# Performance work log

Hardware: AMD Instinct MI355X
Metric: run time of the kernel (lower is better)

The kernel has to match this reference:

```python
import jax, jax.numpy as jnp
import numpy as np

B, S, E = 2, 8192, 128


def setup_inputs() -> dict:
    key = jax.random.key(0)
    ks = jax.random.split(key, 7)
    sc = 1.0 / np.sqrt(E)
    return {
        "x": jax.random.normal(ks[0], (B, S, E), dtype=jnp.float32),
        "Wq": jax.random.normal(ks[1], (E, E), dtype=jnp.float32) * sc,
        "bq": jax.random.normal(ks[2], (E,), dtype=jnp.float32) * 0.01,
        "Wk": jax.random.normal(ks[3], (E, E), dtype=jnp.float32) * sc,
        "bk": jax.random.normal(ks[4], (E,), dtype=jnp.float32) * 0.01,
        "Wv": jax.random.normal(ks[5], (E, E), dtype=jnp.float32) * sc,
        "bv": jax.random.normal(ks[6], (E,), dtype=jnp.float32) * 0.01,
    }


def reference(x, Wq, bq, Wk, bk, Wv, bv):
    # x: [B, S, E]. Conv1d(k=1) == per-slice linear: out[b,s,o] = sum_e W[o,e] x[b,s,e] + b[o]
    embed_dim = x.shape[-1]
    Q = jnp.einsum("bse,oe->bso", x, Wq) + bq  # [B, S, E]
    K = jnp.einsum("bse,oe->bso", x, Wk) + bk
    V = jnp.einsum("bse,oe->bso", x, Wv) + bv
    scores = jnp.einsum("bsd,btd->bst", Q, K) / jnp.sqrt(
        jnp.asarray(embed_dim, dtype=x.dtype)
    )  # [B, S, S]
    A = jax.nn.softmax(scores, axis=-1)
    # torch: out = bmm(V^T_as[B,E,S], A^T)[.transpose] == sum_t A[b,s,t] V[b,t,e]
    out = jnp.einsum("bst,bte->bse", A, V)  # [B, S, E]
    return out
```

## Files before the change

kernel.cpp:

```cpp
#include <hip/hip_runtime.h>
#include <math.h>

#define NB 2
#define NS 8192
#define NE 128
#define NROWS (NB * NS)

typedef __attribute__((ext_vector_type(8))) short s8v;
typedef __attribute__((ext_vector_type(16))) float fx16;
typedef __attribute__((address_space(1))) const unsigned char as1c;
typedef __attribute__((address_space(3))) unsigned char as3t;

static __device__ __forceinline__ unsigned int pkbf(float a, float b) {
    unsigned int ua = __float_as_uint(a), ub = __float_as_uint(b);
    ua += 0x7FFFu + ((ua >> 16) & 1u);
    ub += 0x7FFFu + ((ub >> 16) & 1u);
    return (ua >> 16) | (ub & 0xFFFF0000u);
}

__global__ __launch_bounds__(256, 2)
void qkv_kernel(const float* __restrict__ x,
                const float* __restrict__ Wq, const float* __restrict__ bq,
                const float* __restrict__ Wk, const float* __restrict__ bk,
                const float* __restrict__ Wv, const float* __restrict__ bv,
                unsigned short* __restrict__ qkv)
{
    __shared__ unsigned short WhL[64 * 136];
    __shared__ unsigned short WlL[64 * 136];

    const int t    = threadIdx.x;
    const int rblk = blockIdx.x * 128;
    const int mat  = blockIdx.y;
    const int o0   = blockIdx.z * 64;

    const float* W    = (mat == 0) ? Wq : (mat == 1) ? Wk : Wv;
    const float* bias = (mat == 0) ? bq : (mat == 1) ? bk : bv;
    unsigned short* out = qkv + (size_t)mat * NROWS * NE;
    const float osc = (mat == 0) ? 0.08838834764831845f : 1.0f;

    {
        const int r = t >> 2, cg = (t & 3) * 32;
        #pragma unroll
        for (int j = 0; j < 4; ++j) {
            const float* wp = &W[(size_t)(o0 + r) * NE + cg + j * 8];
            float4 a = *(const float4*)wp;
            float4 b = *(const float4*)(wp + 4);
            unsigned int h0 = pkbf(a.x, a.y), h1 = pkbf(a.z, a.w);
            unsigned int h2 = pkbf(b.x, b.y), h3 = pkbf(b.z, b.w);
            *(uint4*)&WhL[r * 136 + cg + j * 8] = make_uint4(h0, h1, h2, h3);
            float l0 = a.x - __uint_as_float(h0 << 16);
            float l1 = a.y - __uint_as_float(h0 & 0xFFFF0000u);
            float l2 = a.z - __uint_as_float(h1 << 16);
            float l3 = a.w - __uint_as_float(h1 & 0xFFFF0000u);
            float l4 = b.x - __uint_as_float(h2 << 16);
            float l5 = b.y - __uint_as_float(h2 & 0xFFFF0000u);
            float l6 = b.z - __uint_as_float(h3 << 16);
            float l7 = b.w - __uint_as_float(h3 & 0xFFFF0000u);
            *(uint4*)&WlL[r * 136 + cg + j * 8] =
                make_uint4(pkbf(l0, l1), pkbf(l2, l3), pkbf(l4, l5), pkbf(l6, l7));
        }
    }
    __syncthreads();

    const int w = t >> 6, lane = t & 63, lq = lane & 31, h = lane >> 5;
    const int rw = rblk + w * 32;

    s8v xhf[8], xlf[8];
    #pragma unroll
    for (int s = 0; s < 8; ++s) {
        const float* xp = &x[(size_t)(rw + lq) * NE + s * 16 + h * 8];
        float4 a = *(const float4*)xp;
        float4 b = *(const float4*)(xp + 4);
        unsigned int h0 = pkbf(a.x, a.y), h1 = pkbf(a.z, a.w);
        unsigned int h2 = pkbf(b.x, b.y), h3 = pkbf(b.z, b.w);
        float l0 = a.x - __uint_as_float(h0 << 16);
        float l1 = a.y - __uint_as_float(h0 & 0xFFFF0000u);
        float l2 = a.z - __uint_as_float(h1 << 16);
        float l3 = a.w - __uint_as_float(h1 & 0xFFFF0000u);
        float l4 = b.x - __uint_as_float(h2 << 16);
        float l5 = b.y - __uint_as_float(h2 & 0xFFFF0000u);
        float l6 = b.z - __uint_as_float(h3 << 16);
        float l7 = b.w - __uint_as_float(h3 & 0xFFFF0000u);
        union { uint4 u; s8v v; } H, L;
        H.u = make_uint4(h0, h1, h2, h3);
        L.u = make_uint4(pkbf(l0, l1), pkbf(l2, l3), pkbf(l4, l5), pkbf(l6, l7));
        xhf[s] = H.v;
        xlf[s] = L.v;
    }

    fx16 acc[2];
    #pragma unroll
    for (int ot = 0; ot < 2; ++ot)
        #pragma unroll
        for (int i = 0; i < 16; ++i) acc[ot][i] = 0.f;

    #pragma unroll
    for (int s = 0; s < 8; ++s) {
        #pragma unroll
        for (int ot = 0; ot < 2; ++ot) {
            s8v wh = *(const s8v*)&WhL[(ot * 32 + lq) * 136 + s * 16 + h * 8];
            s8v wl = *(const s8v*)&WlL[(ot * 32 + lq) * 136 + s * 16 + h * 8];
            if (mat != 2) {
                acc[ot] = __builtin_amdgcn_mfma_f32_32x32x16_bf16(wh, xhf[s], acc[ot], 0, 0, 0);
                acc[ot] = __builtin_amdgcn_mfma_f32_32x32x16_bf16(wh, xlf[s], acc[ot], 0, 0, 0);
                acc[ot] = __builtin_amdgcn_mfma_f32_32x32x16_bf16(wl, xhf[s], acc[ot], 0, 0, 0);
            } else {
                acc[ot] = __builtin_amdgcn_mfma_f32_32x32x16_bf16(xhf[s], wh, acc[ot], 0, 0, 0);
                acc[ot] = __builtin_amdgcn_mfma_f32_32x32x16_bf16(xlf[s], wh, acc[ot], 0, 0, 0);
                acc[ot] = __builtin_amdgcn_mfma_f32_32x32x16_bf16(xhf[s], wl, acc[ot], 0, 0, 0);
            }
        }
    }

    if (mat != 2) {
        const size_t rbase = (size_t)(rw + lq) * NE;
        #pragma unroll
        for (int ot = 0; ot < 2; ++ot)
            #pragma unroll
            for (int g = 0; g < 4; ++g) {
                int ob = o0 + ot * 32 + 4 * h + 8 * g;
                float4 bb = *(const float4*)&bias[ob];
                float v0 = (acc[ot][4 * g + 0] + bb.x) * osc;
                float v1 = (acc[ot][4 * g + 1] + bb.y) * osc;
                float v2 = (acc[ot][4 * g + 2] + bb.z) * osc;
                float v3 = (acc[ot][4 * g + 3] + bb.w) * osc;
                *(uint2*)&out[rbase + ob] = make_uint2(pkbf(v0, v1), pkbf(v2, v3));
            }
    } else {
        const int bb_ = rw >> 13, kb = (rw & (NS - 1)) + 4 * h;
        #pragma unroll
        for (int ot = 0; ot < 2; ++ot) {
            int o = o0 + ot * 32 + lq;
            float bv = bias[o];
            size_t obase = ((size_t)(bb_ * NE + o) << 13) + kb;
            #pragma unroll
            for (int g = 0; g < 4; ++g) {
                float v0 = acc[ot][4 * g + 0] + bv;
                float v1 = acc[ot][4 * g + 1] + bv;
                float v2 = acc[ot][4 * g + 2] + bv;
                float v3 = acc[ot][4 * g + 3] + bv;
                *(uint2*)&out[obase + 8 * g] = make_uint2(pkbf(v0, v1), pkbf(v2, v3));
            }
        }
    }
}

__global__ __launch_bounds__(256, 2)
void attn_kernel(const unsigned short* __restrict__ qkv,
                 _Float16* __restrict__ pd,
                 _Float16* __restrict__ pw,
                 float* __restrict__ ml)
{
    __shared__ unsigned short kbuf[2][64 * 128];
    __shared__ unsigned short vbuf[2][64 * 128];

    const int t  = threadIdx.x;
    const int id = blockIdx.x;
    const int ks = id & 3;
    const int b  = (id >> 2) & 1;
    const int T  = id >> 3;

    const unsigned short* Qg = qkv;
    const unsigned short* Kg = qkv + (size_t)NROWS * NE;
    const unsigned short* Vb = qkv + (size_t)2 * NROWS * NE + ((size_t)b << 20);

    const int w = t >> 6, lane = t & 63, lq = lane & 31, h = lane >> 5;
    const int qbw = b * NS + T * 128 + w * 32;
    const size_t kvb = (size_t)b * NS * NE;
    const int kq0 = ks * 2048;

    s8v qf[8];
    #pragma unroll
    for (int s = 0; s < 8; ++s)
        qf[s] = *(const s8v*)(Qg + (size_t)(qbw + lq) * NE + s * 16 + h * 8);

    fx16 acc[4];
    #pragma unroll
    for (int dt = 0; dt < 4; ++dt)
        #pragma unroll
        for (int i = 0; i < 16; ++i) acc[dt][i] = 0.f;

    float l = 0.f;

    auto stage = [&](int r, int buf) {
        const int base = kq0 + r * 64;
        if (w < 2) {
            #pragma unroll
            for (int j = 0; j < 8; ++j) {
                int i = 8 * w + j;
                int keyl = 4 * i + (lane >> 4);
                int c = (lane & 15) ^ (keyl & 7);
                const unsigned short* g =
                    Kg + kvb + (size_t)(base + keyl) * NE + c * 8;
                __builtin_amdgcn_global_load_lds((as1c*)g,
                    (as3t*)&kbuf[buf][i * 512], 16, 0, 0);
            }
        } else {
            #pragma unroll
            for (int j = 0; j < 8; ++j) {
                int i = 8 * (w - 2) + j;
                int d = 8 * i + (lane >> 3);
                int g = (lane & 7) ^ (d & 7);
                const unsigned short* gp =
                    Vb + ((size_t)d << 13) + base + g * 8;
                __builtin_amdgcn_global_load_lds((as1c*)gp,
                    (as3t*)&vbuf[buf][i * 512], 16, 0, 0);
            }
        }
    };

    stage(0, 0);
    __syncthreads();

#define PEX(i) (st2[(i) >> 4][(i) & 15])
    int buf = 0;
    const int swz = (lq & 7) * 8;

    for (int r = 0; r < 32; ++r) {
        if (r < 31) stage(r + 1, buf ^ 1);

        fx16 st2[2];
        #pragma unroll
        for (int mt = 0; mt < 2; ++mt)
            #pragma unroll
            for (int i = 0; i < 16; ++i) st2[mt][i] = 0.f;
        #pragma unroll
        for (int s = 0; s < 8; ++s) {
            int co = ((s * 2 + h) * 8) ^ swz;
            s8v a0 = *(const s8v*)&kbuf[buf][lq * 128 + co];
            s8v a1 = *(const s8v*)&kbuf[buf][(32 + lq) * 128 + co];
            st2[0] = __builtin_amdgcn_mfma_f32_32x32x16_bf16(a0, qf[s], st2[0], 0, 0, 0);
            st2[1] = __builtin_amdgcn_mfma_f32_32x32x16_bf16(a1, qf[s], st2[1], 0, 0, 0);
        }

        float lsum = 0.f;
        #pragma unroll
        for (int i = 0; i < 32; ++i) {
            PEX(i) = __expf(PEX(i));
            lsum += PEX(i);
        }
        lsum += __shfl_xor(lsum, 32);
        l += lsum;

        #pragma unroll
        for (int s2 = 0; s2 < 4; ++s2) {
            unsigned int P0 = pkbf(PEX(s2 * 8 + 0), PEX(s2 * 8 + 1));
            unsigned int P1 = pkbf(PEX(s2 * 8 + 2), PEX(s2 * 8 + 3));
            unsigned int P2 = pkbf(PEX(s2 * 8 + 4), PEX(s2 * 8 + 5));
            unsigned int P3 = pkbf(PEX(s2 * 8 + 6), PEX(s2 * 8 + 7));
            unsigned int X0 = (unsigned int)__shfl_xor((int)P0, 32);
            unsigned int X1 = (unsigned int)__shfl_xor((int)P1, 32);
            unsigned int X2 = (unsigned int)__shfl_xor((int)P2, 32);
            unsigned int X3 = (unsigned int)__shfl_xor((int)P3, 32);
            union { unsigned int u[4]; s8v v; } pf;
            pf.u[0] = h ? X2 : P0;
            pf.u[1] = h ? X3 : P1;
            pf.u[2] = h ? P2 : X0;
            pf.u[3] = h ? P3 : X1;
            int go = ((s2 * 2 + h) * 8) ^ swz;
            #pragma unroll
            for (int dt = 0; dt < 4; ++dt) {
                s8v vf = *(const s8v*)&vbuf[buf][(lq + 32 * dt) * 64 + go];
                acc[dt] = __builtin_amdgcn_mfma_f32_32x32x16_bf16(pf.v, vf, acc[dt], 0, 0, 0);
            }
        }

        __syncthreads();
        buf ^= 1;
    }
#undef PEX

    if (lane < 32)
        ml[(size_t)(qbw + lq) * 4 + ks] = l;

    float invl = 1.0f / l;
    _Float16* P = (ks < 2) ? pd : pw;
    const int slot = (ks & 1) * 128;
    #pragma unroll
    for (int rg = 0; rg < 16; ++rg) {
        int row = (rg & 3) + 8 * (rg >> 2) + 4 * h;
        float sc = __shfl(invl, row);
        size_t rb = (size_t)(qbw + row) * 256 + slot;
        #pragma unroll
        for (int dt = 0; dt < 4; ++dt)
            P[rb + lq + 32 * dt] = (_Float16)(acc[dt][rg] * sc);
    }
}

__global__ __launch_bounds__(256, 2)
void merge_kernel(const _Float16* __restrict__ pw,
                  const float* __restrict__ ml,
                  float* __restrict__ outp)
{
    const int gi = blockIdx.x * 256 + threadIdx.x;
    const int q = gi >> 4, d0 = (gi & 15) * 8;
    const _Float16* pd = (const _Float16*)outp;

    uint4 u0 = *(const uint4*)&pd[(size_t)q * 256 + d0];
    uint4 u1 = *(const uint4*)&pd[(size_t)q * 256 + 128 + d0];
    uint4 u2 = *(const uint4*)&pw[(size_t)q * 256 + d0];
    uint4 u3 = *(const uint4*)&pw[(size_t)q * 256 + 128 + d0];
    float l0 = ml[q * 4 + 0], l1 = ml[q * 4 + 1];
    float l2 = ml[q * 4 + 2], l3 = ml[q * 4 + 3];

    float inv = 1.f / (l0 + l1 + l2 + l3);
    float a0 = l0 * inv, a1 = l1 * inv, a2 = l2 * inv, a3 = l3 * inv;

    union { uint4 u; _Float16 hh[8]; } c0, c1, c2, c3;
    c0.u = u0; c1.u = u1; c2.u = u2; c3.u = u3;
    float ov[8];
    #pragma unroll
    for (int e = 0; e < 8; ++e)
        ov[e] = (float)c0.hh[e] * a0 + (float)c1.hh[e] * a1 +
                (float)c2.hh[e] * a2 + (float)c3.hh[e] * a3;

    *(float4*)&outp[(size_t)q * 128 + d0]     = *(float4*)&ov[0];
    *(float4*)&outp[(size_t)q * 128 + d0 + 4] = *(float4*)&ov[4];
}

extern "C" void kernel_launch(void* const* d_in, const int* in_sizes, int n_in,
                              void* d_out, int out_size, void* d_ws, size_t ws_size,
                              hipStream_t stream)
{
    const float* x  = (const float*)d_in[0];
    const float* Wq = (const float*)d_in[1];
    const float* bq = (const float*)d_in[2];
    const float* Wk = (const float*)d_in[3];
    const float* bk = (const float*)d_in[4];
    const float* Wv = (const float*)d_in[5];
    const float* bv = (const float*)d_in[6];
    float* out = (float*)d_out;

    unsigned char* ws = (unsigned char*)d_ws;
    unsigned short* qkv = (unsigned short*)ws;
    _Float16* pw = (_Float16*)(ws + (size_t)3 * NROWS * NE * 2);
    float* mlp = (float*)(ws + (size_t)3 * NROWS * NE * 2
                             + (size_t)NROWS * 256 * 2);

    dim3 g1(NROWS / 128, 3, 2);
    qkv_kernel<<<g1, 256, 0, stream>>>(x, Wq, bq, Wk, bk, Wv, bv, qkv);

    attn_kernel<<<512, 256, 0, stream>>>(qkv, (_Float16*)d_out, pw, mlp);
    merge_kernel<<<1024, 256, 0, stream>>>(pw, mlp, out);
}
```

Before: 171.5 us.

## Fold log2e into Q scale, use exp2, hardware bf16 pack and permlane swap

Folds log2(e) into the Q projection scale so the softmax exponent can use the native exp2 instruction instead of __expf. It replaces the software bf16 rounding with v_cvt_pk_bf16_f32 and the shuffle-plus-select exchange with permlane32_swap. It also precomputes the K/V staging pointers and advances them by a stride, and raises wave priority around the MFMA blocks. The aim is fewer VALU and cross-lane instructions in the inner loop; it relies on gfx950-specific instructions and on the scores staying small enough that skipping max subtraction remains safe.

```diff
diff --git a/kernel.cpp b/kernel.cpp
--- a/kernel.cpp
+++ b/kernel.cpp
@@ -8,6 +8,7 @@
 
 typedef __attribute__((ext_vector_type(8))) short s8v;
 typedef __attribute__((ext_vector_type(16))) float fx16;
+typedef __attribute__((ext_vector_type(2))) unsigned int u2v;
 typedef __attribute__((address_space(1))) const unsigned char as1c;
 typedef __attribute__((address_space(3))) unsigned char as3t;
 
@@ -16,6 +17,12 @@
     ua += 0x7FFFu + ((ua >> 16) & 1u);
     ub += 0x7FFFu + ((ub >> 16) & 1u);
     return (ua >> 16) | (ub & 0xFFFF0000u);
+}
+
+static __device__ __forceinline__ unsigned int cvtpk(float a, float b) {
+    unsigned int r;
+    asm("v_cvt_pk_bf16_f32 %0, %1, %2" : "=v"(r) : "v"(a), "v"(b));
+    return r;
 }
 
 __global__ __launch_bounds__(256, 2)
@@ -36,7 +43,7 @@
     const float* W    = (mat == 0) ? Wq : (mat == 1) ? Wk : Wv;
     const float* bias = (mat == 0) ? bq : (mat == 1) ? bk : bv;
     unsigned short* out = qkv + (size_t)mat * NROWS * NE;
-    const float osc = (mat == 0) ? 0.08838834764831845f : 1.0f;
+    const float osc = (mat == 0) ? 0.1275174460620886f : 1.0f;
 
     {
         const int r = t >> 2, cg = (t & 3) * 32;
@@ -182,34 +189,45 @@
 
     float l = 0.f;
 
-    auto stage = [&](int r, int buf) {
-        const int base = kq0 + r * 64;
+    const unsigned short* gptr[8];
+    if (w < 2) {
+        #pragma unroll
+        for (int j = 0; j < 8; ++j) {
+            int i = 8 * w + j;
+            int keyl = 4 * i + (lane >> 4);
+            int c = (lane & 15) ^ (keyl & 7);
+            gptr[j] = Kg + kvb + (size_t)(kq0 + keyl) * NE + c * 8;
+        }
+    } else {
+        #pragma unroll
+        for (int j = 0; j < 8; ++j) {
+            int i = 8 * (w - 2) + j;
+            int d = 8 * i + (lane >> 3);
+            int g = (lane & 7) ^ (d & 7);
+            gptr[j] = Vb + ((size_t)d << 13) + kq0 + g * 8;
+        }
+    }
+    const int gstride = (w < 2) ? 64 * NE : 64;
+
+    auto stage = [&](int bufi) {
         if (w < 2) {
             #pragma unroll
             for (int j = 0; j < 8; ++j) {
-                int i = 8 * w + j;
-                int keyl = 4 * i + (lane >> 4);
-                int c = (lane & 15) ^ (keyl & 7);
-                const unsigned short* g =
-                    Kg + kvb + (size_t)(base + keyl) * NE + c * 8;
-                __builtin_amdgcn_global_load_lds((as1c*)g,
-                    (as3t*)&kbuf[buf][i * 512], 16, 0, 0);
+                __builtin_amdgcn_global_load_lds((as1c*)gptr[j],
+                    (as3t*)&kbuf[bufi][(8 * w + j) * 512], 16, 0, 0);
+                gptr[j] += gstride;
             }
         } else {
             #pragma unroll
             for (int j = 0; j < 8; ++j) {
-                int i = 8 * (w - 2) + j;
-                int d = 8 * i + (lane >> 3);
-                int g = (lane & 7) ^ (d & 7);
-                const unsigned short* gp =
-                    Vb + ((size_t)d << 13) + base + g * 8;
-                __builtin_amdgcn_global_load_lds((as1c*)gp,
-                    (as3t*)&vbuf[buf][i * 512], 16, 0, 0);
+                __builtin_amdgcn_global_load_lds((as1c*)gptr[j],
+                    (as3t*)&vbuf[bufi][(8 * (w - 2) + j) * 512], 16, 0, 0);
+                gptr[j] += gstride;
             }
         }
     };
 
-    stage(0, 0);
+    stage(0);
     __syncthreads();
 
 #define PEX(i) (st2[(i) >> 4][(i) & 15])
@@ -217,13 +235,14 @@
     const int swz = (lq & 7) * 8;
 
     for (int r = 0; r < 32; ++r) {
-        if (r < 31) stage(r + 1, buf ^ 1);
+        if (r < 31) stage(buf ^ 1);
 
         fx16 st2[2];
         #pragma unroll
         for (int mt = 0; mt < 2; ++mt)
             #pragma unroll
             for (int i = 0; i < 16; ++i) st2[mt][i] = 0.f;
+        __builtin_amdgcn_s_setprio(1);
         #pragma unroll
         for (int s = 0; s < 8; ++s) {
             int co = ((s * 2 + h) * 8) ^ swz;
@@ -232,37 +251,42 @@
             st2[0] = __builtin_amdgcn_mfma_f32_32x32x16_bf16(a0, qf[s], st2[0], 0, 0, 0);
             st2[1] = __builtin_amdgcn_mfma_f32_32x32x16_bf16(a1, qf[s], st2[1], 0, 0, 0);
         }
-
-        float lsum = 0.f;
-        #pragma unroll
-        for (int i = 0; i < 32; ++i) {
-            PEX(i) = __expf(PEX(i));
-            lsum += PEX(i);
-        }
+        __builtin_amdgcn_s_setprio(0);
+
+        float a0s = 0.f, a1s = 0.f, a2s = 0.f, a3s = 0.f;
+        #pragma unroll
+        for (int i = 0; i < 32; i += 4) {
+            PEX(i)     = __builtin_amdgcn_exp2f(PEX(i));
+            PEX(i + 1) = __builtin_amdgcn_exp2f(PEX(i + 1));
+            PEX(i + 2) = __builtin_amdgcn_exp2f(PEX(i + 2));
+            PEX(i + 3) = __builtin_amdgcn_exp2f(PEX(i + 3));
+            a0s += PEX(i); a1s += PEX(i + 1); a2s += PEX(i + 2); a3s += PEX(i + 3);
+        }
+        float lsum = (a0s + a1s) + (a2s + a3s);
         lsum += __shfl_xor(lsum, 32);
         l += lsum;
 
         #pragma unroll
         for (int s2 = 0; s2 < 4; ++s2) {
-            unsigned int P0 = pkbf(PEX(s2 * 8 + 0), PEX(s2 * 8 + 1));
-            unsigned int P1 = pkbf(PEX(s2 * 8 + 2), PEX(s2 * 8 + 3));
-            unsigned int P2 = pkbf(PEX(s2 * 8 + 4), PEX(s2 * 8 + 5));
-            unsigned int P3 = pkbf(PEX(s2 * 8 + 6), PEX(s2 * 8 + 7));
-            unsigned int X0 = (unsigned int)__shfl_xor((int)P0, 32);
-            unsigned int X1 = (unsigned int)__shfl_xor((int)P1, 32);
-            unsigned int X2 = (unsigned int)__shfl_xor((int)P2, 32);
-            unsigned int X3 = (unsigned int)__shfl_xor((int)P3, 32);
+            unsigned int P0 = cvtpk(PEX(s2 * 8 + 0), PEX(s2 * 8 + 1));
+            unsigned int P1 = cvtpk(PEX(s2 * 8 + 2), PEX(s2 * 8 + 3));
+            unsigned int P2 = cvtpk(PEX(s2 * 8 + 4), PEX(s2 * 8 + 5));
+            unsigned int P3 = cvtpk(PEX(s2 * 8 + 6), PEX(s2 * 8 + 7));
+            u2v r02 = __builtin_amdgcn_permlane32_swap(P0, P2, false, false);
+            u2v r13 = __builtin_amdgcn_permlane32_swap(P1, P3, false, false);
             union { unsigned int u[4]; s8v v; } pf;
-            pf.u[0] = h ? X2 : P0;
-            pf.u[1] = h ? X3 : P1;
-            pf.u[2] = h ? P2 : X0;
-            pf.u[3] = h ? P3 : X1;
+            pf.u[0] = r02.x;
+            pf.u[1] = r13.x;
+            pf.u[2] = r02.y;
+            pf.u[3] = r13.y;
             int go = ((s2 * 2 + h) * 8) ^ swz;
+            __builtin_amdgcn_s_setprio(1);
             #pragma unroll
             for (int dt = 0; dt < 4; ++dt) {
                 s8v vf = *(const s8v*)&vbuf[buf][(lq + 32 * dt) * 64 + go];
                 acc[dt] = __builtin_amdgcn_mfma_f32_32x32x16_bf16(pf.v, vf, acc[dt], 0, 0, 0);
             }
+            __builtin_amdgcn_s_setprio(0);
         }
 
         __syncthreads();
```

After: 163.7 us. 4.5% less time.
